# Optimization experiments

Hardware: AMD Instinct MI355X
Metric: run time of the kernel (lower is better)

The kernel has to match this reference:

```python
import jax, jax.numpy as jnp
import numpy as np

B, N, T, S = 32, 102400, 64, 1600
PI = float(np.pi)
EPS = 1e-12  # numerical guard inside sqrt for cdist (diagonal is exactly 0)


def _cdist(a, b):
    # a: (..., P, 3), b: (..., Q, 3) -> (..., P, Q) euclidean distances
    sq = jnp.sum((a[..., :, None, :] - b[..., None, :, :]) ** 2, axis=-1)
    return jnp.sqrt(sq + EPS)


def _rigid_t(alpha, trans, sz, center):
    # alpha, trans: (B, T, 3). Returns XYZ (B,T,3,3), translation (B,T,3).
    c, s = jnp.cos(alpha), jnp.sin(alpha)
    z = jnp.zeros_like(c[..., 0]); o = jnp.ones_like(c[..., 0])
    X = jnp.stack([c[..., 0], -s[..., 0], z, s[..., 0], c[..., 0], z, z, z, o], -1).reshape(*alpha.shape[:2], 3, 3)
    Y = jnp.stack([c[..., 1], z, s[..., 1], z, o, z, -s[..., 1], z, c[..., 1]], -1).reshape(*alpha.shape[:2], 3, 3)
    Z = jnp.stack([o, z, z, z, c[..., 2], -s[..., 2], z, s[..., 2], c[..., 2]], -1).reshape(*alpha.shape[:2], 3, 3)
    XYZ = jnp.einsum('btij,btjk,btkl->btil', X, Y, Z)
    eye = jnp.eye(3, dtype=alpha.dtype)
    Tt = trans * sz[None, None, :] + jnp.einsum('m,btmk->btk', center, eye[None, None] - XYZ)
    return XYZ, Tt


def setup_inputs():
    key = jax.random.key(0)
    ks = jax.random.split(key, 6)
    x = jax.random.normal(ks[0], (B, 6, N), jnp.float32)
    w1 = jax.random.normal(ks[1], (3 * N, 32), jnp.float32) * 0.005
    b1 = jnp.zeros((32,), jnp.float32)
    w2 = jax.random.normal(ks[2], (32, 6 * T), jnp.float32) * 0.05
    b2 = jnp.zeros((6 * T,), jnp.float32)
    A = jax.random.normal(ks[3], (6, N), jnp.float32)
    mask = jax.random.uniform(ks[4], (T, T), jnp.float32)
    sz = jnp.array([128.0, 128.0, 64.0], jnp.float32)
    tess = jnp.arange(N, dtype=jnp.int32).reshape(T, S)  # equal-size partition
    return {'x': x, 'w1': w1, 'b1': b1, 'w2': w2, 'b2': b2, 'A': A, 'mask': mask, 'sz': sz, 'tess': tess}


def reference(x, w1, b1, w2, b2, A, mask, sz, tess):
    center = sz / 2.0
    # localization MLP on flattened xyz coords: (B, 3N) -> (B, T, 6)
    xflat = x[:, :3, :].reshape(B, 3 * N)
    h = jax.nn.relu(xflat @ w1 + b1)
    z_l = jnp.tanh(h @ w2 + b2).reshape(B, T, 6)
    # NOTE: original code uses z_l[:, :, 3:] for BOTH angles and translation
    r_, t_ = _rigid_t(PI * z_l[:, :, 3:], z_l[:, :, 3:], sz, center)
    x3 = x[:, :3, :]
    xg = x3[:, :, tess]  # gather: (B, 3, T, S)
    # out[b,j,p,n] = sum_k r_[b,p,k,j] * xg[b,k,p,n]  (matches einsum 'bkt,bkn->btn')
    rot = jnp.einsum('bpkj,bkpn->bjpn', r_, xg) + t_.transpose(0, 2, 1)[:, :, :, None]
    # scatter back into full point cloud (tess partitions N)
    X3 = jnp.zeros_like(x3).at[:, :, tess.reshape(-1)].set(rot.reshape(B, 3, N))
    X_t = jnp.concatenate([X3, x[:, 3:, :]], axis=1)  # colors pass through identity
    # regularizer on per-piece centroids
    pts_1 = A[:3][:, tess].mean(axis=2).T                 # (T, 3)
    pts_2 = X3[:, :, tess].mean(axis=3).transpose(0, 2, 1)  # (B, T, 3)
    diff = _cdist(pts_1, pts_1)[None] - _cdist(pts_2, pts_2)
    reg = jnp.sum((mask[None] * diff) ** 2, axis=(1, 2))  # (B,)
    return X_t, reg
```

## Files before the change

### kernel.cpp

```cpp
#include <hip/hip_runtime.h>
#include <hip/hip_bf16.h>
#include <math.h>

#define BB 32
#define NN 102400
#define TT 64
#define SS 1600
#define K3N (3 * NN)
#define KC 64
#define G1 512
#define CPB 512
#define NCHUNK (K3N / KC)
#define XP 68
#define WP 40
#define PI_F 3.14159265358979323846f

__global__ __launch_bounds__(256) void k1_mega(const float* __restrict__ x,
                                               const float* __restrict__ w1,
                                               const float* __restrict__ A,
                                               const int* __restrict__ tess,
                                               float* __restrict__ h_part,
                                               float* __restrict__ out,
                                               float* __restrict__ pts1) {
    const int tid = threadIdx.x;
    if (blockIdx.x < G1) {
        __shared__ float xs[2][32 * XP];
        __shared__ float ws1[2][KC * WP];
        const int ks = tid & 7;
        const int tile = tid >> 3;
        const int bg = tile & 7;
        const int cg = tile >> 3;
        const int sxb = tid >> 4, sxk = (tid & 15) * 4;
        const int swr = tid >> 3, swc = (tid & 7) * 4;

        float acc[4][8];
        #pragma unroll
        for (int j = 0; j < 4; ++j)
            #pragma unroll
            for (int c = 0; c < 8; ++c) acc[j][c] = 0.f;

        const int start = (int)(((long)blockIdx.x * NCHUNK) / G1);
        const int end   = (int)(((long)(blockIdx.x + 1) * NCHUNK) / G1);

        float4 rx0, rx1, rw0, rw1;
        {
            const int k0 = start * KC;
            rx0 = *(const float4*)(x + (size_t)sxb * 6 * NN + k0 + sxk);
            rx1 = *(const float4*)(x + (size_t)(sxb + 16) * 6 * NN + k0 + sxk);
            rw0 = *(const float4*)(w1 + (size_t)(k0 + swr) * 32 + swc);
            rw1 = *(const float4*)(w1 + (size_t)(k0 + swr + 32) * 32 + swc);
            *(float4*)(xs[0] + sxb * XP + sxk) = rx0;
            *(float4*)(xs[0] + (sxb + 16) * XP + sxk) = rx1;
            *(float4*)(ws1[0] + swr * WP + swc) = rw0;
            *(float4*)(ws1[0] + (swr + 32) * WP + swc) = rw1;
        }
        __syncthreads();

        int cur = 0;
        for (int chunk = start; chunk < end; ++chunk) {
            const bool more = (chunk + 1) < end;
            if (more) {
                const int k0 = (chunk + 1) * KC;
                rx0 = *(const float4*)(x + (size_t)sxb * 6 * NN + k0 + sxk);
                rx1 = *(const float4*)(x + (size_t)(sxb + 16) * 6 * NN + k0 + sxk);
                rw0 = *(const float4*)(w1 + (size_t)(k0 + swr) * 32 + swc);
                rw1 = *(const float4*)(w1 + (size_t)(k0 + swr + 32) * 32 + swc);
            }
            const float* xc = xs[cur];
            const float* wc = ws1[cur];
            #pragma unroll
            for (int i = 0; i < 8; ++i) {
                const int k = ks + 8 * i;
                const float4 wa = *(const float4*)(wc + k * WP + cg * 8);
                const float4 wb = *(const float4*)(wc + k * WP + cg * 8 + 4);
                float xv[4];
                #pragma unroll
                for (int j = 0; j < 4; ++j) xv[j] = xc[(bg + 8 * j) * XP + k];
                #pragma unroll
                for (int j = 0; j < 4; ++j) {
                    acc[j][0] = fmaf(xv[j], wa.x, acc[j][0]);
                    acc[j][1] = fmaf(xv[j], wa.y, acc[j][1]);
                    acc[j][2] = fmaf(xv[j], wa.z, acc[j][2]);
                    acc[j][3] = fmaf(xv[j], wa.w, acc[j][3]);
                    acc[j][4] = fmaf(xv[j], wb.x, acc[j][4]);
                    acc[j][5] = fmaf(xv[j], wb.y, acc[j][5]);
                    acc[j][6] = fmaf(xv[j], wb.z, acc[j][6]);
                    acc[j][7] = fmaf(xv[j], wb.w, acc[j][7]);
                }
            }
            if (more) {
                const int nb = cur ^ 1;
                *(float4*)(xs[nb] + sxb * XP + sxk) = rx0;
                *(float4*)(xs[nb] + (sxb + 16) * XP + sxk) = rx1;
                *(float4*)(ws1[nb] + swr * WP + swc) = rw0;
                *(float4*)(ws1[nb] + (swr + 32) * WP + swc) = rw1;
            }
            __syncthreads();
            cur ^= 1;
        }

        #pragma unroll
        for (int off = 1; off < 8; off <<= 1) {
            #pragma unroll
            for (int j = 0; j < 4; ++j)
                #pragma unroll
                for (int c = 0; c < 8; ++c)
                    acc[j][c] += __shfl_xor(acc[j][c], off, 64);
        }
        if (ks == 0) {
            float* hp = h_part + (size_t)blockIdx.x * 1024;
            #pragma unroll
            for (int j = 0; j < 4; ++j) {
                const int b = bg + 8 * j;
                #pragma unroll
                for (int c = 0; c < 8; ++c)
                    hp[b * 32 + cg * 8 + c] = acc[j][c];
            }
        }
    } else if (blockIdx.x < G1 + CPB) {
        const int cb = blockIdx.x - G1;
        for (long i = (long)cb * 256 + tid; i < 2457600L; i += (long)CPB * 256) {
            const int b = (int)(i / 76800);
            const int rem = (int)(i - (long)b * 76800);
            const size_t off = (size_t)b * (6 * NN) + K3N + (size_t)rem * 4;
            *(float4*)(out + off) = *(const float4*)(x + off);
        }
    } else {
        const int t = blockIdx.x - G1 - CPB;
        const int* tr = tess + t * SS;
        float s0 = 0.f, s1 = 0.f, s2 = 0.f;
        for (int s = tid; s < SS; s += 256) {
            const int idx = tr[s];
            s0 += A[idx]; s1 += A[NN + idx]; s2 += A[2 * NN + idx];
        }
        #pragma unroll
        for (int o = 32; o > 0; o >>= 1) {
            s0 += __shfl_down(s0, o, 64);
            s1 += __shfl_down(s1, o, 64);
            s2 += __shfl_down(s2, o, 64);
        }
        __shared__ float red[4 * 3];
        const int lane = tid & 63, wv = tid >> 6;
        if (lane == 0) { red[wv * 3] = s0; red[wv * 3 + 1] = s1; red[wv * 3 + 2] = s2; }
        __syncthreads();
        if (tid < 3) {
            const float s = red[tid] + red[3 + tid] + red[6 + tid] + red[9 + tid];
            pts1[t * 3 + tid] = s * (1.0f / SS);
        }
    }
}

__global__ __launch_bounds__(256) void kb_rigid(const float* __restrict__ h_part,
                                                const float* __restrict__ b1,
                                                const float* __restrict__ w2,
                                                const float* __restrict__ b2,
                                                const float* __restrict__ sz,
                                                float* __restrict__ RT) {
    const int bb = blockIdx.x;
    __shared__ float part[8][32];
    __shared__ float hsh[32];
    const int c = threadIdx.x & 31, g = threadIdx.x >> 5;
    float s = 0.f;
    for (int j = g; j < G1; j += 8) s += h_part[(size_t)j * 1024 + bb * 32 + c];
    part[g][c] = s;
    __syncthreads();
    if (threadIdx.x < 32) {
        float acc = 0.f;
        #pragma unroll
        for (int g2 = 0; g2 < 8; ++g2) acc += part[g2][threadIdx.x];
        hsh[threadIdx.x] = fmaxf(acc + b1[threadIdx.x], 0.f);
    }
    __syncthreads();
    const int t = threadIdx.x;
    if (t < TT) {
        float z[3];
        #pragma unroll
        for (int j = 0; j < 3; ++j) {
            const int col = 6 * t + 3 + j;
            float s2 = b2[col];
            #pragma unroll 8
            for (int cc = 0; cc < 32; ++cc) s2 = fmaf(hsh[cc], w2[cc * 384 + col], s2);
            z[j] = tanhf(s2);
        }
        float c0, s0, c1, s1, c2, s2v;
        sincosf(PI_F * z[0], &s0, &c0);
        sincosf(PI_F * z[1], &s1, &c1);
        sincosf(PI_F * z[2], &s2v, &c2);
        const float R00 = c0 * c1;
        const float R01 = -s0 * c2 + c0 * s1 * s2v;
        const float R02 = s0 * s2v + c0 * s1 * c2;
        const float R10 = s0 * c1;
        const float R11 = c0 * c2 + s0 * s1 * s2v;
        const float R12 = -c0 * s2v + s0 * s1 * c2;
        const float R20 = -s1;
        const float R21 = c1 * s2v;
        const float R22 = c1 * c2;
        const float szx = sz[0], szy = sz[1], szz = sz[2];
        const float cx = 0.5f * szx, cy = 0.5f * szy, cz = 0.5f * szz;
        const float T0 = z[0] * szx + cx - (cx * R00 + cy * R10 + cz * R20);
        const float T1 = z[1] * szy + cy - (cx * R01 + cy * R11 + cz * R21);
        const float T2 = z[2] * szz + cz - (cx * R02 + cy * R12 + cz * R22);
        float* o = RT + (bb * TT + t) * 12;
        o[0] = R00; o[1] = R10; o[2]  = R20; o[3]  = T0;
        o[4] = R01; o[5] = R11; o[6]  = R21; o[7]  = T1;
        o[8] = R02; o[9] = R12; o[10] = R22; o[11] = T2;
    }
}

__global__ __launch_bounds__(256) void k3_transform(const float* __restrict__ x,
                                                    const int* __restrict__ tess,
                                                    const float* __restrict__ RT,
                                                    float* __restrict__ out,
                                                    float* __restrict__ pts2) {
    const int blk = blockIdx.x;
    const int b = blk / TT, t = blk % TT;
    const float* p = RT + blk * 12;
    const float M00 = p[0], M01 = p[1], M02 = p[2], T0 = p[3];
    const float M10 = p[4], M11 = p[5], M12 = p[6], T1 = p[7];
    const float M20 = p[8], M21 = p[9], M22 = p[10], T2 = p[11];
    const float* xb = x + (size_t)b * 6 * NN;
    float* ob = out + (size_t)b * 6 * NN;
    const int* tr = tess + t * SS;
    float s0 = 0.f, s1 = 0.f, s2 = 0.f;
    for (int s = threadIdx.x; s < SS; s += 256) {
        const int idx = tr[s];
        const float x0 = xb[idx], x1 = xb[NN + idx], x2 = xb[2 * NN + idx];
        const float y0 = fmaf(M00, x0, fmaf(M01, x1, fmaf(M02, x2, T0)));
        const float y1 = fmaf(M10, x0, fmaf(M11, x1, fmaf(M12, x2, T1)));
        const float y2 = fmaf(M20, x0, fmaf(M21, x1, fmaf(M22, x2, T2)));
        ob[idx] = y0; ob[NN + idx] = y1; ob[2 * NN + idx] = y2;
        s0 += y0; s1 += y1; s2 += y2;
    }
    #pragma unroll
    for (int o = 32; o > 0; o >>= 1) {
        s0 += __shfl_down(s0, o, 64);
        s1 += __shfl_down(s1, o, 64);
        s2 += __shfl_down(s2, o, 64);
    }
    __shared__ float red[4 * 3];
    const int lane = threadIdx.x & 63, wv = threadIdx.x >> 6;
    if (lane == 0) { red[wv * 3] = s0; red[wv * 3 + 1] = s1; red[wv * 3 + 2] = s2; }
    __syncthreads();
    if (threadIdx.x < 3) {
        const float s = red[threadIdx.x] + red[3 + threadIdx.x] + red[6 + threadIdx.x] + red[9 + threadIdx.x];
        pts2[blk * 3 + threadIdx.x] = s * (1.0f / SS);
    }
}

__global__ __launch_bounds__(256) void k5_reg(const float* __restrict__ pts1,
                                              const float* __restrict__ pts2,
                                              const float* __restrict__ mask,
                                              float* __restrict__ out) {
    const int b = blockIdx.x;
    __shared__ float p1[TT * 3], p2[TT * 3];
    for (int i = threadIdx.x; i < TT * 3; i += 256) {
        p1[i] = pts1[i];
        p2[i] = pts2[b * TT * 3 + i];
    }
    __syncthreads();
    float acc = 0.f;
    for (int pr = threadIdx.x; pr < TT * TT; pr += 256) {
        const int t = pr >> 6, u = pr & 63;
        float dx = p1[t * 3] - p1[u * 3];
        float dy = p1[t * 3 + 1] - p1[u * 3 + 1];
        float dz = p1[t * 3 + 2] - p1[u * 3 + 2];
        const float d1 = sqrtf(dx * dx + dy * dy + dz * dz + 1e-12f);
        dx = p2[t * 3] - p2[u * 3];
        dy = p2[t * 3 + 1] - p2[u * 3 + 1];
        dz = p2[t * 3 + 2] - p2[u * 3 + 2];
        const float d2 = sqrtf(dx * dx + dy * dy + dz * dz + 1e-12f);
        const float d = mask[pr] * (d1 - d2);
        acc = fmaf(d, d, acc);
    }
    #pragma unroll
    for (int o = 32; o > 0; o >>= 1) acc += __shfl_down(acc, o, 64);
    __shared__ float red[4];
    const int lane = threadIdx.x & 63, wv = threadIdx.x >> 6;
    if (lane == 0) red[wv] = acc;
    __syncthreads();
    if (threadIdx.x == 0) {
        out[(size_t)BB * 6 * NN + b] = red[0] + red[1] + red[2] + red[3];
    }
}

extern "C" void kernel_launch(void* const* d_in, const int* in_sizes, int n_in,
                              void* d_out, int out_size, void* d_ws, size_t ws_size,
                              hipStream_t stream) {
    const float* x    = (const float*)d_in[0];
    const float* w1   = (const float*)d_in[1];
    const float* b1   = (const float*)d_in[2];
    const float* w2   = (const float*)d_in[3];
    const float* b2   = (const float*)d_in[4];
    const float* A    = (const float*)d_in[5];
    const float* mask = (const float*)d_in[6];
    const float* sz   = (const float*)d_in[7];
    const int*   tess = (const int*)d_in[8];
    float* out = (float*)d_out;
    float* ws  = (float*)d_ws;

    float* h_part = ws;
    float* RT     = h_part + (size_t)G1 * 1024;
    float* pts2   = RT + BB * TT * 12;
    float* pts1   = pts2 + BB * TT * 3;

    k1_mega<<<G1 + CPB + TT, 256, 0, stream>>>(x, w1, A, tess, h_part, out, pts1);
    kb_rigid<<<BB, 256, 0, stream>>>(h_part, b1, w2, b2, sz, RT);
    k3_transform<<<BB * TT, 256, 0, stream>>>(x, tess, RT, out, pts2);
    k5_reg<<<BB, 256, 0, stream>>>(pts1, pts2, mask, out);
}
```

Baseline: 74.64 us.

## Stream w1 directly from global, swizzle x tile in LDS, double GEMV split

The skinny GEMV stage no longer stages w1 through shared memory. Each thread reads its own contiguous 8x8 slice of w1 straight from global, and the x tile is held in LDS with an XOR swizzle so each thread can load vectorized float4 rows without bank conflicts. The split-K block count goes from 512 to a runtime value of up to 1024, capped by workspace size, to put more bytes in flight. The cost is more partial sums for the reduction kernel to add up, and uncoalesced per-thread w1 reads that now depend on cache behaviour.

```diff
diff --git a/kernel.cpp b/kernel.cpp
--- a/kernel.cpp
+++ b/kernel.cpp
@@ -8,11 +8,8 @@
 #define SS 1600
 #define K3N (3 * NN)
 #define KC 64
-#define G1 512
 #define CPB 512
 #define NCHUNK (K3N / KC)
-#define XP 68
-#define WP 40
 #define PI_F 3.14159265358979323846f
 
 __global__ __launch_bounds__(256) void k1_mega(const float* __restrict__ x,
@@ -21,17 +18,22 @@
                                                const int* __restrict__ tess,
                                                float* __restrict__ h_part,
                                                float* __restrict__ out,
-                                               float* __restrict__ pts1) {
+                                               float* __restrict__ pts1,
+                                               int g1) {
     const int tid = threadIdx.x;
-    if (blockIdx.x < G1) {
-        __shared__ float xs[2][32 * XP];
-        __shared__ float ws1[2][KC * WP];
-        const int ks = tid & 7;
-        const int tile = tid >> 3;
-        const int bg = tile & 7;
-        const int cg = tile >> 3;
-        const int sxb = tid >> 4, sxk = (tid & 15) * 4;
-        const int swr = tid >> 3, swc = (tid & 7) * 4;
+    if (blockIdx.x < g1) {
+        __shared__ float xs[2][32 * 64];
+        const int ksOwn = tid & 7;
+        const int bg = (tid >> 3) & 7;
+        const int cg = tid >> 6;
+        const int r0 = tid >> 4, c40 = tid & 15;
+        const int r1 = (tid + 256) >> 4, c41 = tid & 15;
+        const int l0 = r0 * 64 + ((c40 ^ (r0 & 7)) << 2);
+        const int l1 = r1 * 64 + ((c41 ^ (r1 & 7)) << 2);
+        const size_t gx0 = (size_t)r0 * 6 * NN + 4 * c40;
+        const size_t gx1 = (size_t)r1 * 6 * NN + 4 * c41;
+        const int sA = ((2 * ksOwn) ^ bg) << 2;
+        const int sB = ((2 * ksOwn + 1) ^ bg) << 2;
 
         float acc[4][8];
         #pragma unroll
@@ -39,20 +41,16 @@
             #pragma unroll
             for (int c = 0; c < 8; ++c) acc[j][c] = 0.f;
 
-        const int start = (int)(((long)blockIdx.x * NCHUNK) / G1);
-        const int end   = (int)(((long)(blockIdx.x + 1) * NCHUNK) / G1);
-
-        float4 rx0, rx1, rw0, rw1;
+        const int start = (int)(((long)blockIdx.x * NCHUNK) / g1);
+        const int end   = (int)(((long)(blockIdx.x + 1) * NCHUNK) / g1);
+
+        float4 rxA, rxB;
         {
             const int k0 = start * KC;
-            rx0 = *(const float4*)(x + (size_t)sxb * 6 * NN + k0 + sxk);
-            rx1 = *(const float4*)(x + (size_t)(sxb + 16) * 6 * NN + k0 + sxk);
-            rw0 = *(const float4*)(w1 + (size_t)(k0 + swr) * 32 + swc);
-            rw1 = *(const float4*)(w1 + (size_t)(k0 + swr + 32) * 32 + swc);
-            *(float4*)(xs[0] + sxb * XP + sxk) = rx0;
-            *(float4*)(xs[0] + (sxb + 16) * XP + sxk) = rx1;
-            *(float4*)(ws1[0] + swr * WP + swc) = rw0;
-            *(float4*)(ws1[0] + (swr + 32) * WP + swc) = rw1;
+            rxA = *(const float4*)(x + gx0 + k0);
+            rxB = *(const float4*)(x + gx1 + k0);
+            *(float4*)(xs[0] + l0) = rxA;
+            *(float4*)(xs[0] + l1) = rxB;
         }
         __syncthreads();
 
@@ -60,40 +58,42 @@
         for (int chunk = start; chunk < end; ++chunk) {
             const bool more = (chunk + 1) < end;
             if (more) {
-                const int k0 = (chunk + 1) * KC;
-                rx0 = *(const float4*)(x + (size_t)sxb * 6 * NN + k0 + sxk);
-                rx1 = *(const float4*)(x + (size_t)(sxb + 16) * 6 * NN + k0 + sxk);
-                rw0 = *(const float4*)(w1 + (size_t)(k0 + swr) * 32 + swc);
-                rw1 = *(const float4*)(w1 + (size_t)(k0 + swr + 32) * 32 + swc);
+                const int k0n = (chunk + 1) * KC;
+                rxA = *(const float4*)(x + gx0 + k0n);
+                rxB = *(const float4*)(x + gx1 + k0n);
             }
             const float* xc = xs[cur];
-            const float* wc = ws1[cur];
-            #pragma unroll
-            for (int i = 0; i < 8; ++i) {
-                const int k = ks + 8 * i;
-                const float4 wa = *(const float4*)(wc + k * WP + cg * 8);
-                const float4 wb = *(const float4*)(wc + k * WP + cg * 8 + 4);
-                float xv[4];
-                #pragma unroll
-                for (int j = 0; j < 4; ++j) xv[j] = xc[(bg + 8 * j) * XP + k];
+            float4 xa[4], xb[4];
+            #pragma unroll
+            for (int j = 0; j < 4; ++j) {
+                const int base = (bg + 8 * j) * 64;
+                xa[j] = *(const float4*)(xc + base + sA);
+                xb[j] = *(const float4*)(xc + base + sB);
+            }
+            const float* wrow = w1 + (size_t)(chunk * KC + 8 * ksOwn) * 32 + cg * 8;
+            #pragma unroll
+            for (int kk = 0; kk < 8; ++kk) {
+                const float4 wa = *(const float4*)(wrow + kk * 32);
+                const float4 wb = *(const float4*)(wrow + kk * 32 + 4);
                 #pragma unroll
                 for (int j = 0; j < 4; ++j) {
-                    acc[j][0] = fmaf(xv[j], wa.x, acc[j][0]);
-                    acc[j][1] = fmaf(xv[j], wa.y, acc[j][1]);
-                    acc[j][2] = fmaf(xv[j], wa.z, acc[j][2]);
-                    acc[j][3] = fmaf(xv[j], wa.w, acc[j][3]);
-                    acc[j][4] = fmaf(xv[j], wb.x, acc[j][4]);
-                    acc[j][5] = fmaf(xv[j], wb.y, acc[j][5]);
-                    acc[j][6] = fmaf(xv[j], wb.z, acc[j][6]);
-                    acc[j][7] = fmaf(xv[j], wb.w, acc[j][7]);
+                    const float xj = kk < 4
+                        ? (kk == 0 ? xa[j].x : (kk == 1 ? xa[j].y : (kk == 2 ? xa[j].z : xa[j].w)))
+                        : (kk == 4 ? xb[j].x : (kk == 5 ? xb[j].y : (kk == 6 ? xb[j].z : xb[j].w)));
+                    acc[j][0] = fmaf(xj, wa.x, acc[j][0]);
+                    acc[j][1] = fmaf(xj, wa.y, acc[j][1]);
+                    acc[j][2] = fmaf(xj, wa.z, acc[j][2]);
+                    acc[j][3] = fmaf(xj, wa.w, acc[j][3]);
+                    acc[j][4] = fmaf(xj, wb.x, acc[j][4]);
+                    acc[j][5] = fmaf(xj, wb.y, acc[j][5]);
+                    acc[j][6] = fmaf(xj, wb.z, acc[j][6]);
+                    acc[j][7] = fmaf(xj, wb.w, acc[j][7]);
                 }
             }
             if (more) {
-                const int nb = cur ^ 1;
-                *(float4*)(xs[nb] + sxb * XP + sxk) = rx0;
-                *(float4*)(xs[nb] + (sxb + 16) * XP + sxk) = rx1;
-                *(float4*)(ws1[nb] + swr * WP + swc) = rw0;
-                *(float4*)(ws1[nb] + (swr + 32) * WP + swc) = rw1;
+                float* xn = xs[cur ^ 1];
+                *(float4*)(xn + l0) = rxA;
+                *(float4*)(xn + l1) = rxB;
             }
             __syncthreads();
             cur ^= 1;
@@ -107,7 +107,7 @@
                 for (int c = 0; c < 8; ++c)
                     acc[j][c] += __shfl_xor(acc[j][c], off, 64);
         }
-        if (ks == 0) {
+        if (ksOwn == 0) {
             float* hp = h_part + (size_t)blockIdx.x * 1024;
             #pragma unroll
             for (int j = 0; j < 4; ++j) {
@@ -117,16 +117,16 @@
                     hp[b * 32 + cg * 8 + c] = acc[j][c];
             }
         }
-    } else if (blockIdx.x < G1 + CPB) {
-        const int cb = blockIdx.x - G1;
-        for (long i = (long)cb * 256 + tid; i < 2457600L; i += (long)CPB * 256) {
-            const int b = (int)(i / 76800);
-            const int rem = (int)(i - (long)b * 76800);
+    } else if (blockIdx.x < g1 + CPB) {
+        const int cb = blockIdx.x - g1;
+        for (int i = cb * 256 + tid; i < 2457600; i += CPB * 256) {
+            const int b = i / 76800;
+            const int rem = i - b * 76800;
             const size_t off = (size_t)b * (6 * NN) + K3N + (size_t)rem * 4;
             *(float4*)(out + off) = *(const float4*)(x + off);
         }
     } else {
-        const int t = blockIdx.x - G1 - CPB;
+        const int t = blockIdx.x - g1 - CPB;
         const int* tr = tess + t * SS;
         float s0 = 0.f, s1 = 0.f, s2 = 0.f;
         for (int s = tid; s < SS; s += 256) {
@@ -155,13 +155,14 @@
                                                 const float* __restrict__ w2,
                                                 const float* __restrict__ b2,
                                                 const float* __restrict__ sz,
-                                                float* __restrict__ RT) {
+                                                float* __restrict__ RT,
+                                                int g1) {
     const int bb = blockIdx.x;
     __shared__ float part[8][32];
     __shared__ float hsh[32];
     const int c = threadIdx.x & 31, g = threadIdx.x >> 5;
     float s = 0.f;
-    for (int j = g; j < G1; j += 8) s += h_part[(size_t)j * 1024 + bb * 32 + c];
+    for (int j = g; j < g1; j += 8) s += h_part[(size_t)j * 1024 + bb * 32 + c];
     part[g][c] = s;
     __syncthreads();
     if (threadIdx.x < 32) {
@@ -298,13 +299,16 @@
     float* out = (float*)d_out;
     float* ws  = (float*)d_ws;
 
+    int g1 = 1024;
+    while ((size_t)((size_t)g1 * 1024 + 2048 * 12 + 2048 * 3 + 192) * 4 > ws_size && g1 > 128) g1 >>= 1;
+
     float* h_part = ws;
-    float* RT     = h_part + (size_t)G1 * 1024;
+    float* RT     = h_part + (size_t)g1 * 1024;
     float* pts2   = RT + BB * TT * 12;
     float* pts1   = pts2 + BB * TT * 3;
 
-    k1_mega<<<G1 + CPB + TT, 256, 0, stream>>>(x, w1, A, tess, h_part, out, pts1);
-    kb_rigid<<<BB, 256, 0, stream>>>(h_part, b1, w2, b2, sz, RT);
+    k1_mega<<<g1 + CPB + TT, 256, 0, stream>>>(x, w1, A, tess, h_part, out, pts1, g1);
+    kb_rigid<<<BB, 256, 0, stream>>>(h_part, b1, w2, b2, sz, RT, g1);
     k3_transform<<<BB * TT, 256, 0, stream>>>(x, tess, RT, out, pts2);
     k5_reg<<<BB, 256, 0, stream>>>(pts1, pts2, mask, out);
 }
```

Result: slower. 116.5 us (+56.0%).
